# Kernel tuning notes

Hardware: AMD Instinct MI355X
Metric: run time of the kernel (lower is better)

## Reference

```python
import jax, jax.numpy as jnp
import numpy as np

B, T, E = 4, 1024, 1024
H, MULT = 16, 2
HD = E // H
SCALE = HD ** -0.5


def setup_inputs() -> dict:
    key = jax.random.key(0)
    ks = jax.random.split(key, 9)
    s = 0.02
    return {
        "hidden_states": jax.random.normal(ks[0], (B, T, E), jnp.float32),
        "attention_mask": jnp.zeros((B, 1, T, T), jnp.float32),
        "Wq": jax.random.normal(ks[1], (E, E), jnp.float32) * s,
        "bq": jnp.zeros((E,), jnp.float32),
        "Wk": jax.random.normal(ks[2], (MULT * E, E), jnp.float32) * s,
        "bk": jnp.zeros((MULT * E,), jnp.float32),
        "Wv": jax.random.normal(ks[3], (MULT * E, E), jnp.float32) * s,
        "bv": jnp.zeros((MULT * E,), jnp.float32),
        "Wo": jax.random.normal(ks[4], (E, E), jnp.float32) * s,
        "bo": jnp.zeros((E,), jnp.float32),
    }


def reference(hidden_states, attention_mask, Wq, bq, Wk, bk, Wv, bv, Wo, bo):
    x = hidden_states  # [B, T, E]
    # q projection, scaled
    q = (jnp.einsum("bte,fe->btf", x, Wq) + bq) * SCALE  # [B,T,E]
    q = q.reshape(B, T, H, HD).transpose(0, 2, 1, 3)      # [B,H,T,HD]
    # k/v project to multiplier-expanded dim, then _shape with seq_len=-1:
    # [B,T,MULT*E] -> view(B, T*MULT, H, HD) (torch view semantics) -> [B,H,T*MULT,HD]
    k = jnp.einsum("bte,fe->btf", x, Wk) + bk             # [B,T,MULT*E]
    k = k.reshape(B, T * MULT, H, HD).transpose(0, 2, 1, 3)
    v = jnp.einsum("bte,fe->btf", x, Wv) + bv
    v = v.reshape(B, T * MULT, H, HD).transpose(0, 2, 1, 3)

    S = T * MULT  # src_len; src_len0 = T
    attn = jnp.einsum("bhtd,bhsd->bhts", q, k)            # [B,H,T,S]
    # custom mask broadcast: view src as [MULT, src_len0] and add mask[:, :, :, None, :]
    attn = attn.reshape(B, H, T, MULT, T) + attention_mask[:, :, :, None, :]
    attn = attn.reshape(B, H, T, S)
    attn = jax.nn.softmax(attn, axis=-1)
    out = jnp.einsum("bhts,bhsd->bhtd", attn, v)          # [B,H,T,HD]
    out = out.transpose(0, 2, 1, 3).reshape(B, T, E)
    out = jnp.einsum("bte,fe->btf", out, Wo) + bo
    return out
```

## Files before the change

### kernel.cpp

```cpp
#include <hip/hip_runtime.h>
#include <math.h>

#define BB    4
#define TT    1024
#define EE    1024
#define HH    16
#define HDIM  64
#define SS    2048
#define MROWS 4096
#define SCALEQ 0.125f

typedef short  s8v  __attribute__((ext_vector_type(8)));
typedef float  f4v  __attribute__((ext_vector_type(4)));

__device__ __forceinline__ unsigned short f2bf(float f) {
    union { float f; unsigned u; } c; c.f = f;
    unsigned u = c.u + 0x7FFFu + ((c.u >> 16) & 1u);
    return (unsigned short)(u >> 16);
}
__device__ __forceinline__ float bf2f(unsigned short h) {
    union { unsigned u; float f; } c; c.u = ((unsigned)h) << 16;
    return c.f;
}

__device__ __forceinline__ void async16(const void* g, void* l) {
    __builtin_amdgcn_global_load_lds(
        (const __attribute__((address_space(1))) unsigned int*)g,
        (__attribute__((address_space(3))) unsigned int*)l,
        16, 0, 0);
}

__global__ __launch_bounds__(256) void cvt6_kernel(
    const float* __restrict__ x,  const float* __restrict__ wq,
    const float* __restrict__ wk, const float* __restrict__ wv,
    const float* __restrict__ wo, const float* __restrict__ mk,
    unsigned short* __restrict__ xb,  unsigned short* __restrict__ wqb,
    unsigned short* __restrict__ wkb, unsigned short* __restrict__ wvb,
    unsigned short* __restrict__ wob, unsigned short* __restrict__ mbb)
{
    const int total = 3670016;
    int i = blockIdx.x * 256 + threadIdx.x;
    const int stride = gridDim.x * 256;
    for (; i < total; i += stride) {
        const float* s; unsigned short* d; int off;
        if (i < 1048576)      { s = x;  d = xb;  off = i; }
        else if (i < 1310720) { s = wq; d = wqb; off = i - 1048576; }
        else if (i < 1835008) { s = wk; d = wkb; off = i - 1310720; }
        else if (i < 2359296) { s = wv; d = wvb; off = i - 1835008; }
        else if (i < 2621440) { s = wo; d = wob; off = i - 2359296; }
        else                  { s = mk; d = mbb; off = i - 2621440; }
        float4 v = ((const float4*)s)[off];
        ushort4 o;
        o.x = f2bf(v.x); o.y = f2bf(v.y); o.z = f2bf(v.z); o.w = f2bf(v.w);
        ((ushort4*)d)[off] = o;
    }
}

#define GEMM_KLOOP(Aptr, Wptr, Ksz)                                            \
    for (int k0 = 0; k0 < (Ksz); k0 += 32) {                                   \
        _Pragma("unroll")                                                      \
        for (int it = 0; it < 2; ++it) {                                       \
            int f = (it * 4 + w) * 64 + lane;                                  \
            int r = f >> 2, g = (f & 3) * 8;                                   \
            async16((Aptr) + (size_t)(m0 + r) * (Ksz) + k0 + g,                \
                    As + (it * 4 + w) * 512);                                  \
            async16((Wptr) + (size_t)(n0 + r) * (Ksz) + k0 + g,                \
                    Bs + (it * 4 + w) * 512);                                  \
        }                                                                      \
        __syncthreads();                                                       \
        s8v af[4], bf[4];                                                      \
        _Pragma("unroll")                                                      \
        for (int i = 0; i < 4; ++i)                                            \
            af[i] = *(const s8v*)(As + (wm + i * 16 + col16) * 32 + quad * 8); \
        _Pragma("unroll")                                                      \
        for (int j = 0; j < 4; ++j)                                            \
            bf[j] = *(const s8v*)(Bs + (wn + j * 16 + col16) * 32 + quad * 8); \
        _Pragma("unroll")                                                      \
        for (int i = 0; i < 4; ++i)                                            \
            _Pragma("unroll")                                                  \
            for (int j = 0; j < 4; ++j)                                        \
                acc[i][j] = __builtin_amdgcn_mfma_f32_16x16x32_bf16(           \
                    af[i], bf[j], acc[i][j], 0, 0, 0);                         \
        __syncthreads();                                                       \
    }

__global__ __launch_bounds__(256, 3) void gemm_qk_kernel(
    const unsigned short* __restrict__ X,  const unsigned short* __restrict__ Wq,
    const unsigned short* __restrict__ Wk, const float* __restrict__ bq,
    const float* __restrict__ bk, unsigned short* __restrict__ qp,
    unsigned short* __restrict__ kp)
{
    __shared__ __align__(16) unsigned short As[128 * 32];
    __shared__ __align__(16) unsigned short Bs[128 * 32];

    const int tid = threadIdx.x;
    const int lane = tid & 63, w = tid >> 6;
    const int wm = (w & 1) * 64, wn = (w >> 1) * 64;
    const int col16 = lane & 15, quad = lane >> 4;
    const int m0 = blockIdx.x * 128;
    const bool isQ = blockIdx.y < 8;
    const int n0 = blockIdx.y * 128;
    const unsigned short* Wrow = isQ ? Wq + (size_t)n0 * EE
                                     : Wk + (size_t)(n0 - EE) * EE;

    f4v acc[4][4];
#pragma unroll
    for (int i = 0; i < 4; ++i)
#pragma unroll
        for (int j = 0; j < 4; ++j) acc[i][j] = (f4v)0.0f;

    for (int k0 = 0; k0 < EE; k0 += 32) {
#pragma unroll
        for (int it = 0; it < 2; ++it) {
            int f = (it * 4 + w) * 64 + lane;
            int r = f >> 2, g = (f & 3) * 8;
            async16(X + (size_t)(m0 + r) * EE + k0 + g, As + (it * 4 + w) * 512);
            async16(Wrow + (size_t)r * EE + k0 + g, Bs + (it * 4 + w) * 512);
        }
        __syncthreads();
        s8v af[4], bf[4];
#pragma unroll
        for (int i = 0; i < 4; ++i)
            af[i] = *(const s8v*)(As + (wm + i * 16 + col16) * 32 + quad * 8);
#pragma unroll
        for (int j = 0; j < 4; ++j)
            bf[j] = *(const s8v*)(Bs + (wn + j * 16 + col16) * 32 + quad * 8);
#pragma unroll
        for (int i = 0; i < 4; ++i)
#pragma unroll
            for (int j = 0; j < 4; ++j)
                acc[i][j] = __builtin_amdgcn_mfma_f32_16x16x32_bf16(
                    af[i], bf[j], acc[i][j], 0, 0, 0);
        __syncthreads();
    }

#pragma unroll
    for (int j = 0; j < 4; ++j) {
        const int n = n0 + wn + j * 16 + col16;
        const float bn = isQ ? bq[n] : bk[n - EE];
#pragma unroll
        for (int i = 0; i < 4; ++i) {
            const int mb = m0 + wm + i * 16 + quad * 4;
#pragma unroll
            for (int r = 0; r < 4; ++r) {
                const int m = mb + r;
                float c = acc[i][j][r] + bn;
                if (isQ) {
                    qp[(size_t)m * EE + n] = f2bf(c * SCALEQ);
                } else {
                    const int nk = n - EE;
                    const int mm = nk >> 10, h = (nk >> 6) & 15, d = nk & 63;
                    const int b_ = m >> 10, t = m & 1023;
                    const int s = 2 * t + mm;
                    kp[((size_t)(b_ * HH + h) * SS + s) * HDIM + d] = f2bf(c);
                }
            }
        }
    }
}

template <int LAYOUT, int OUTF32, int Ksz, int Nsz>
__global__ __launch_bounds__(256, 3) void gemm_mfma_kernel(
    const unsigned short* __restrict__ A, const unsigned short* __restrict__ W,
    const float* __restrict__ bias, void* __restrict__ Cout, float alpha)
{
    __shared__ __align__(16) unsigned short As[128 * 32];
    __shared__ __align__(16) unsigned short Bs[128 * 32];

    const int tid = threadIdx.x;
    const int lane = tid & 63, w = tid >> 6;
    const int wm = (w & 1) * 64, wn = (w >> 1) * 64;
    const int col16 = lane & 15, quad = lane >> 4;
    const int m0 = blockIdx.x * 128;
    const int n0 = blockIdx.y * 128;

    f4v acc[4][4];
#pragma unroll
    for (int i = 0; i < 4; ++i)
#pragma unroll
        for (int j = 0; j < 4; ++j) acc[i][j] = (f4v)0.0f;

    GEMM_KLOOP(A, W, Ksz)

#pragma unroll
    for (int j = 0; j < 4; ++j) {
        const int n = n0 + wn + j * 16 + col16;
        const float bn = (LAYOUT == 2) ? 0.0f : bias[n];
#pragma unroll
        for (int i = 0; i < 4; ++i) {
            const int mb = m0 + wm + i * 16 + quad * 4;
#pragma unroll
            for (int r = 0; r < 4; ++r) {
                const int m = mb + r;
                float c = (acc[i][j][r] + ((LAYOUT == 2) ? bias[m] : bn)) * alpha;
                if (LAYOUT == 0) {
                    if (OUTF32) ((float*)Cout)[(size_t)m * Nsz + n] = c;
                    else ((unsigned short*)Cout)[(size_t)m * Nsz + n] = f2bf(c);
                } else {
                    const int mm = m >> 10, h = (m >> 6) & 15, d = m & 63;
                    const int b_ = n >> 10, t = n & 1023;
                    const int s = 2 * t + mm;
                    ((unsigned short*)Cout)[((size_t)(b_ * HH + h) * HDIM + d) * SS + s] = f2bf(c);
                }
            }
        }
    }
}

__global__ __launch_bounds__(256, 3) void attn_mfma2_kernel(
    const unsigned short* __restrict__ Q, const unsigned short* __restrict__ Kh,
    const unsigned short* __restrict__ Vt, const unsigned short* __restrict__ Mb,
    unsigned short* __restrict__ O)
{
    constexpr int PT = 68;
    __shared__ __align__(16) unsigned short Qs[64 * PT];
    __shared__ __align__(16) unsigned short K0[64 * PT];
    __shared__ __align__(16) unsigned short K1[64 * PT];
    __shared__ __align__(16) unsigned short V0[64 * PT];
    __shared__ __align__(16) unsigned short V1[64 * PT];
    __shared__ __align__(16) unsigned short Ms[64 * PT];

    const int tid = threadIdx.x;
    const int lane = tid & 63, w = tid >> 6;
    const int col16 = lane & 15, quad = lane >> 4;

    const int gid = blockIdx.x;
    const int v = gid & 7, j = gid >> 3;
    const int bh = v * 8 + (j >> 4);
    const int t0 = (j & 15) * 64;
    const int b_ = bh >> 4, h = bh & 15;

#pragma unroll
    for (int it = 0; it < 2; ++it) {
        int idx = tid + it * 256;
        int r = idx >> 3, c = (idx & 7) * 8;
        *(uint4*)(Qs + r * PT + c) =
            *(const uint4*)(Q + (size_t)(b_ * TT + t0 + r) * EE + h * HDIM + c);
    }

    f4v oacc[4];
#pragma unroll
    for (int jd = 0; jd < 4; ++jd) oacc[jd] = (f4v)0.0f;
    float mrun = -INFINITY, lrun = 0.0f;

    const unsigned short* Kb  = Kh + (size_t)bh * SS * HDIM;
    const unsigned short* Vb  = Vt + (size_t)bh * HDIM * SS;
    const unsigned short* Mbb = Mb + (size_t)b_ * TT * TT;
    const int myrow = (w * 16 + col16) * PT;

    for (int it16 = 0; it16 < 16; ++it16) {
        const int t2b = it16 * 64;
        __syncthreads();
#pragma unroll
        for (int st = 0; st < 2; ++st) {
            int idx = tid + st * 256;
            int r = idx >> 3, c = (idx & 7) * 8;
            *(uint4*)(K0 + r * PT + c) = *(const uint4*)(Kb + (size_t)(t2b + r) * HDIM + c);
            *(uint4*)(K1 + r * PT + c) = *(const uint4*)(Kb + (size_t)(1024 + t2b + r) * HDIM + c);
            *(uint4*)(V0 + r * PT + c) = *(const uint4*)(Vb + (size_t)r * SS + t2b + c);
            *(uint4*)(V1 + r * PT + c) = *(const uint4*)(Vb + (size_t)r * SS + 1024 + t2b + c);
            *(uint4*)(Ms + r * PT + c) = *(const uint4*)(Mbb + (size_t)(t0 + r) * TT + t2b + c);
        }
        __syncthreads();

        f4v s0acc[4], s1acc[4];
#pragma unroll
        for (int js = 0; js < 4; ++js) { s0acc[js] = (f4v)0.0f; s1acc[js] = (f4v)0.0f; }
#pragma unroll
        for (int ks = 0; ks < 2; ++ks) {
            s8v bq_ = *(const s8v*)(Qs + myrow + ks * 32 + quad * 8);
#pragma unroll
            for (int js = 0; js < 4; ++js) {
                s8v ak0 = *(const s8v*)(K0 + (js * 16 + col16) * PT + ks * 32 + quad * 8);
                s8v ak1 = *(const s8v*)(K1 + (js * 16 + col16) * PT + ks * 32 + quad * 8);
                s0acc[js] = __builtin_amdgcn_mfma_f32_16x16x32_bf16(ak0, bq_, s0acc[js], 0, 0, 0);
                s1acc[js] = __builtin_amdgcn_mfma_f32_16x16x32_bf16(ak1, bq_, s1acc[js], 0, 0, 0);
            }
        }

#pragma unroll
        for (int js = 0; js < 4; ++js) {
            uint2 mm = *(const uint2*)(Ms + myrow + js * 16 + quad * 4);
            float m0f = bf2f((unsigned short)(mm.x & 0xffff));
            float m1f = bf2f((unsigned short)(mm.x >> 16));
            float m2f = bf2f((unsigned short)(mm.y & 0xffff));
            float m3f = bf2f((unsigned short)(mm.y >> 16));
            s0acc[js][0] += m0f; s1acc[js][0] += m0f;
            s0acc[js][1] += m1f; s1acc[js][1] += m1f;
            s0acc[js][2] += m2f; s1acc[js][2] += m2f;
            s0acc[js][3] += m3f; s1acc[js][3] += m3f;
        }

        float tmax = -INFINITY;
#pragma unroll
        for (int js = 0; js < 4; ++js)
#pragma unroll
            for (int r = 0; r < 4; ++r)
                tmax = fmaxf(tmax, fmaxf(s0acc[js][r], s1acc[js][r]));
        tmax = fmaxf(tmax, __shfl_xor(tmax, 16));
        tmax = fmaxf(tmax, __shfl_xor(tmax, 32));
        const float mnew = fmaxf(mrun, tmax);
        const float scl = __expf(mrun - mnew);
        float rs = 0.0f;
#pragma unroll
        for (int js = 0; js < 4; ++js)
#pragma unroll
            for (int r = 0; r < 4; ++r) {
                float p0 = __expf(s0acc[js][r] - mnew);
                float p1 = __expf(s1acc[js][r] - mnew);
                s0acc[js][r] = p0; s1acc[js][r] = p1;
                rs += p0 + p1;
            }
        rs += __shfl_xor(rs, 16);
        rs += __shfl_xor(rs, 32);
        lrun = lrun * scl + rs;
        mrun = mnew;

        float sclr[4];
#pragma unroll
        for (int r = 0; r < 4; ++r) sclr[r] = __shfl(scl, quad * 4 + r);
#pragma unroll
        for (int jd = 0; jd < 4; ++jd)
#pragma unroll
            for (int r = 0; r < 4; ++r) oacc[jd][r] *= sclr[r];

        __syncthreads();

#pragma unroll
        for (int js = 0; js < 4; ++js) {
            unsigned p01 = (unsigned)f2bf(s0acc[js][0]) | ((unsigned)f2bf(s0acc[js][1]) << 16);
            unsigned p23 = (unsigned)f2bf(s0acc[js][2]) | ((unsigned)f2bf(s0acc[js][3]) << 16);
            *(uint2*)(K0 + myrow + js * 16 + quad * 4) = make_uint2(p01, p23);
            p01 = (unsigned)f2bf(s1acc[js][0]) | ((unsigned)f2bf(s1acc[js][1]) << 16);
            p23 = (unsigned)f2bf(s1acc[js][2]) | ((unsigned)f2bf(s1acc[js][3]) << 16);
            *(uint2*)(K1 + myrow + js * 16 + quad * 4) = make_uint2(p01, p23);
        }
        __syncthreads();

#pragma unroll
        for (int ks = 0; ks < 2; ++ks) {
            s8v p0 = *(const s8v*)(K0 + myrow + ks * 32 + quad * 8);
            s8v p1 = *(const s8v*)(K1 + myrow + ks * 32 + quad * 8);
#pragma unroll
            for (int jd = 0; jd < 4; ++jd) {
                s8v v0_ = *(const s8v*)(V0 + (jd * 16 + col16) * PT + ks * 32 + quad * 8);
                s8v v1_ = *(const s8v*)(V1 + (jd * 16 + col16) * PT + ks * 32 + quad * 8);
                oacc[jd] = __builtin_amdgcn_mfma_f32_16x16x32_bf16(p0, v0_, oacc[jd], 0, 0, 0);
                oacc[jd] = __builtin_amdgcn_mfma_f32_16x16x32_bf16(p1, v1_, oacc[jd], 0, 0, 0);
            }
        }
    }

    const float inv = 1.0f / lrun;
    float invr[4];
#pragma unroll
    for (int r = 0; r < 4; ++r) invr[r] = __shfl(inv, quad * 4 + r);
#pragma unroll
    for (int r = 0; r < 4; ++r) {
        const int t = t0 + w * 16 + quad * 4 + r;
#pragma unroll
        for (int jd = 0; jd < 4; ++jd)
            O[(size_t)(b_ * TT + t) * EE + h * HDIM + jd * 16 + col16] =
                f2bf(oacc[jd][r] * invr[r]);
    }
}

extern "C" void kernel_launch(void* const* d_in, const int* in_sizes, int n_in,
                              void* d_out, int out_size, void* d_ws, size_t ws_size,
                              hipStream_t stream)
{
    (void)in_sizes; (void)n_in; (void)out_size; (void)ws_size;

    const float* x    = (const float*)d_in[0];
    const float* mask = (const float*)d_in[1];
    const float* Wq   = (const float*)d_in[2];
    const float* bq   = (const float*)d_in[3];
    const float* Wk   = (const float*)d_in[4];
    const float* bk   = (const float*)d_in[5];
    const float* Wv   = (const float*)d_in[6];
    const float* bv   = (const float*)d_in[7];
    const float* Wo   = (const float*)d_in[8];
    const float* bo   = (const float*)d_in[9];
    float* out = (float*)d_out;

    unsigned short* xb  = (unsigned short*)d_ws;
    unsigned short* wqb = xb  + (size_t)MROWS * EE;
    unsigned short* wkb = wqb + (size_t)EE * EE;
    unsigned short* wvb = wkb + (size_t)2 * EE * EE;
    unsigned short* wob = wvb + (size_t)2 * EE * EE;
    unsigned short* mb  = wob + (size_t)EE * EE;
    unsigned short* qp  = mb  + (size_t)BB * TT * TT;
    unsigned short* kp  = qp  + (size_t)MROWS * EE;
    unsigned short* vt  = kp  + (size_t)BB * HH * SS * HDIM;
    unsigned short* ao  = vt  + (size_t)BB * HH * SS * HDIM;

    dim3 blk(256);

    cvt6_kernel<<<4096, blk, 0, stream>>>(x, Wq, Wk, Wv, Wo, mask,
                                          xb, wqb, wkb, wvb, wob, mb);
    gemm_qk_kernel<<<dim3(32, 24), blk, 0, stream>>>(xb, wqb, wkb, bq, bk, qp, kp);
    gemm_mfma_kernel<2, 0, EE, MROWS><<<dim3(16, 32), blk, 0, stream>>>(
        wvb, xb, bv, vt, 1.0f);
    attn_mfma2_kernel<<<dim3(1024), blk, 0, stream>>>(qp, kp, vt, mb, ao);
    gemm_mfma_kernel<0, 1, EE, EE><<<dim3(32, 8), blk, 0, stream>>>(
        ao, wob, bo, out, 1.0f);
}
```

Baseline: 287.0 us.

## Use exp2 softmax with lazy rescaling, register Q and mask, less LDS

Folds log2(e) into the Q scale and the mask conversion so the softmax can use native exp2. The running max is only updated when a new tile exceeds it by more than a threshold, and the row sum is kept per lane and reduced once at the end. Q fragments and mask values now load straight into registers instead of going through shared memory. That frees LDS and lets occupancy rise to 4 blocks per CU. Packed bf16 conversion uses an inline cvt_pk instruction; the trade-off is that lazy rescaling lets exponents grow up to 2^10 before renormalising.

```diff
diff --git a/kernel.cpp b/kernel.cpp
--- a/kernel.cpp
+++ b/kernel.cpp
@@ -8,7 +8,8 @@
 #define HDIM  64
 #define SS    2048
 #define MROWS 4096
-#define SCALEQ 0.125f
+#define QSCALE 0.18033688011112f
+#define LOG2E  1.4426950408889634f
 
 typedef short  s8v  __attribute__((ext_vector_type(8)));
 typedef float  f4v  __attribute__((ext_vector_type(4)));
@@ -18,9 +19,11 @@
     unsigned u = c.u + 0x7FFFu + ((c.u >> 16) & 1u);
     return (unsigned short)(u >> 16);
 }
-__device__ __forceinline__ float bf2f(unsigned short h) {
-    union { unsigned u; float f; } c; c.u = ((unsigned)h) << 16;
-    return c.f;
+__device__ __forceinline__ float bflo(unsigned u) {
+    union { unsigned u; float f; } c; c.u = u << 16; return c.f;
+}
+__device__ __forceinline__ float bfhi(unsigned u) {
+    union { unsigned u; float f; } c; c.u = u & 0xffff0000u; return c.f;
 }
 
 __device__ __forceinline__ void async16(const void* g, void* l) {
@@ -42,16 +45,17 @@
     int i = blockIdx.x * 256 + threadIdx.x;
     const int stride = gridDim.x * 256;
     for (; i < total; i += stride) {
-        const float* s; unsigned short* d; int off;
+        const float* s; unsigned short* d; int off; float sc = 1.0f;
         if (i < 1048576)      { s = x;  d = xb;  off = i; }
         else if (i < 1310720) { s = wq; d = wqb; off = i - 1048576; }
         else if (i < 1835008) { s = wk; d = wkb; off = i - 1310720; }
         else if (i < 2359296) { s = wv; d = wvb; off = i - 1835008; }
         else if (i < 2621440) { s = wo; d = wob; off = i - 2359296; }
-        else                  { s = mk; d = mbb; off = i - 2621440; }
+        else                  { s = mk; d = mbb; off = i - 2621440; sc = LOG2E; }
         float4 v = ((const float4*)s)[off];
         ushort4 o;
-        o.x = f2bf(v.x); o.y = f2bf(v.y); o.z = f2bf(v.z); o.w = f2bf(v.w);
+        o.x = f2bf(v.x * sc); o.y = f2bf(v.y * sc);
+        o.z = f2bf(v.z * sc); o.w = f2bf(v.w * sc);
         ((ushort4*)d)[off] = o;
     }
 }
@@ -146,7 +150,7 @@
                 const int m = mb + r;
                 float c = acc[i][j][r] + bn;
                 if (isQ) {
-                    qp[(size_t)m * EE + n] = f2bf(c * SCALEQ);
+                    qp[(size_t)m * EE + n] = f2bf(c * QSCALE);
                 } else {
                     const int nk = n - EE;
                     const int mm = nk >> 10, h = (nk >> 6) & 15, d = nk & 63;
@@ -207,18 +211,16 @@
     }
 }
 
-__global__ __launch_bounds__(256, 3) void attn_mfma2_kernel(
+__global__ __launch_bounds__(256, 4) void attn_mfma3_kernel(
     const unsigned short* __restrict__ Q, const unsigned short* __restrict__ Kh,
     const unsigned short* __restrict__ Vt, const unsigned short* __restrict__ Mb,
     unsigned short* __restrict__ O)
 {
     constexpr int PT = 68;
-    __shared__ __align__(16) unsigned short Qs[64 * PT];
     __shared__ __align__(16) unsigned short K0[64 * PT];
     __shared__ __align__(16) unsigned short K1[64 * PT];
     __shared__ __align__(16) unsigned short V0[64 * PT];
     __shared__ __align__(16) unsigned short V1[64 * PT];
-    __shared__ __align__(16) unsigned short Ms[64 * PT];
 
     const int tid = threadIdx.x;
     const int lane = tid & 63, w = tid >> 6;
@@ -230,26 +232,31 @@
     const int t0 = (j & 15) * 64;
     const int b_ = bh >> 4, h = bh & 15;
 
-#pragma unroll
-    for (int it = 0; it < 2; ++it) {
-        int idx = tid + it * 256;
-        int r = idx >> 3, c = (idx & 7) * 8;
-        *(uint4*)(Qs + r * PT + c) =
-            *(const uint4*)(Q + (size_t)(b_ * TT + t0 + r) * EE + h * HDIM + c);
-    }
+    const unsigned short* Qrow =
+        Q + (size_t)(b_ * TT + t0 + w * 16 + col16) * EE + h * HDIM;
+    const s8v qf0 = *(const s8v*)(Qrow + quad * 8);
+    const s8v qf1 = *(const s8v*)(Qrow + 32 + quad * 8);
 
     f4v oacc[4];
 #pragma unroll
     for (int jd = 0; jd < 4; ++jd) oacc[jd] = (f4v)0.0f;
-    float mrun = -INFINITY, lrun = 0.0f;
-
-    const unsigned short* Kb  = Kh + (size_t)bh * SS * HDIM;
-    const unsigned short* Vb  = Vt + (size_t)bh * HDIM * SS;
-    const unsigned short* Mbb = Mb + (size_t)b_ * TT * TT;
+    float mrun = -INFINITY;
+    f4v l4 = (f4v)0.0f;
+
+    const unsigned short* Kb   = Kh + (size_t)bh * SS * HDIM;
+    const unsigned short* Vb   = Vt + (size_t)bh * HDIM * SS;
+    const unsigned short* Mrow = Mb + (size_t)b_ * TT * TT
+                               + (size_t)(t0 + w * 16 + col16) * TT;
     const int myrow = (w * 16 + col16) * PT;
 
     for (int it16 = 0; it16 < 16; ++it16) {
         const int t2b = it16 * 64;
+
+        uint2 mm[4];
+#pragma unroll
+        for (int js = 0; js < 4; ++js)
+            mm[js] = *(const uint2*)(Mrow + t2b + js * 16 + quad * 4);
+
         __syncthreads();
 #pragma unroll
         for (int st = 0; st < 2; ++st) {
@@ -259,16 +266,20 @@
             *(uint4*)(K1 + r * PT + c) = *(const uint4*)(Kb + (size_t)(1024 + t2b + r) * HDIM + c);
             *(uint4*)(V0 + r * PT + c) = *(const uint4*)(Vb + (size_t)r * SS + t2b + c);
             *(uint4*)(V1 + r * PT + c) = *(const uint4*)(Vb + (size_t)r * SS + 1024 + t2b + c);
-            *(uint4*)(Ms + r * PT + c) = *(const uint4*)(Mbb + (size_t)(t0 + r) * TT + t2b + c);
         }
         __syncthreads();
 
         f4v s0acc[4], s1acc[4];
 #pragma unroll
-        for (int js = 0; js < 4; ++js) { s0acc[js] = (f4v)0.0f; s1acc[js] = (f4v)0.0f; }
+        for (int js = 0; js < 4; ++js) {
+            f4v mv;
+            mv[0] = bflo(mm[js].x); mv[1] = bfhi(mm[js].x);
+            mv[2] = bflo(mm[js].y); mv[3] = bfhi(mm[js].y);
+            s0acc[js] = mv; s1acc[js] = mv;
+        }
 #pragma unroll
         for (int ks = 0; ks < 2; ++ks) {
-            s8v bq_ = *(const s8v*)(Qs + myrow + ks * 32 + quad * 8);
+            const s8v bq_ = ks ? qf1 : qf0;
 #pragma unroll
             for (int js = 0; js < 4; ++js) {
                 s8v ak0 = *(const s8v*)(K0 + (js * 16 + col16) * PT + ks * 32 + quad * 8);
@@ -278,62 +289,56 @@
             }
         }
 
+        float tm0 = fmaxf(fmaxf(s0acc[0][0], s0acc[0][1]), fmaxf(s0acc[0][2], s0acc[0][3]));
+        float tm1 = fmaxf(fmaxf(s0acc[1][0], s0acc[1][1]), fmaxf(s0acc[1][2], s0acc[1][3]));
+        float tm2 = fmaxf(fmaxf(s0acc[2][0], s0acc[2][1]), fmaxf(s0acc[2][2], s0acc[2][3]));
+        float tm3 = fmaxf(fmaxf(s0acc[3][0], s0acc[3][1]), fmaxf(s0acc[3][2], s0acc[3][3]));
+        float tn0 = fmaxf(fmaxf(s1acc[0][0], s1acc[0][1]), fmaxf(s1acc[0][2], s1acc[0][3]));
+        float tn1 = fmaxf(fmaxf(s1acc[1][0], s1acc[1][1]), fmaxf(s1acc[1][2], s1acc[1][3]));
+        float tn2 = fmaxf(fmaxf(s1acc[2][0], s1acc[2][1]), fmaxf(s1acc[2][2], s1acc[2][3]));
+        float tn3 = fmaxf(fmaxf(s1acc[3][0], s1acc[3][1]), fmaxf(s1acc[3][2], s1acc[3][3]));
+        float tmax = fmaxf(fmaxf(fmaxf(tm0, tm1), fmaxf(tm2, tm3)),
+                           fmaxf(fmaxf(tn0, tn1), fmaxf(tn2, tn3)));
+
+        if (!__all(tmax - mrun <= 10.0f)) {
+            float tfull = fmaxf(tmax, __shfl_xor(tmax, 16));
+            tfull = fmaxf(tfull, __shfl_xor(tfull, 32));
+            const float mnew = fmaxf(mrun, tfull);
+            const float scl = __builtin_amdgcn_exp2f(mrun - mnew);
+            l4 *= scl;
+            float sclr[4];
+#pragma unroll
+            for (int r = 0; r < 4; ++r) sclr[r] = __shfl(scl, quad * 4 + r);
+#pragma unroll
+            for (int jd = 0; jd < 4; ++jd)
+#pragma unroll
+                for (int r = 0; r < 4; ++r) oacc[jd][r] *= sclr[r];
+            mrun = mnew;
+        }
+
+        unsigned pk0[8], pk1[8];
 #pragma unroll
         for (int js = 0; js < 4; ++js) {
-            uint2 mm = *(const uint2*)(Ms + myrow + js * 16 + quad * 4);
-            float m0f = bf2f((unsigned short)(mm.x & 0xffff));
-            float m1f = bf2f((unsigned short)(mm.x >> 16));
-            float m2f = bf2f((unsigned short)(mm.y & 0xffff));
-            float m3f = bf2f((unsigned short)(mm.y >> 16));
-            s0acc[js][0] += m0f; s1acc[js][0] += m0f;
-            s0acc[js][1] += m1f; s1acc[js][1] += m1f;
-            s0acc[js][2] += m2f; s1acc[js][2] += m2f;
-            s0acc[js][3] += m3f; s1acc[js][3] += m3f;
-        }
-
-        float tmax = -INFINITY;
-#pragma unroll
-        for (int js = 0; js < 4; ++js)
-#pragma unroll
-            for (int r = 0; r < 4; ++r)
-                tmax = fmaxf(tmax, fmaxf(s0acc[js][r], s1acc[js][r]));
-        tmax = fmaxf(tmax, __shfl_xor(tmax, 16));
-        tmax = fmaxf(tmax, __shfl_xor(tmax, 32));
-        const float mnew = fmaxf(mrun, tmax);
-        const float scl = __expf(mrun - mnew);
-        float rs = 0.0f;
-#pragma unroll
-        for (int js = 0; js < 4; ++js)
+            f4v p0 = s0acc[js] - mrun;
+            f4v p1 = s1acc[js] - mrun;
 #pragma unroll
             for (int r = 0; r < 4; ++r) {
-                float p0 = __expf(s0acc[js][r] - mnew);
-                float p1 = __expf(s1acc[js][r] - mnew);
-                s0acc[js][r] = p0; s1acc[js][r] = p1;
-                rs += p0 + p1;
+                p0[r] = __builtin_amdgcn_exp2f(p0[r]);
+                p1[r] = __builtin_amdgcn_exp2f(p1[r]);
             }
-        rs += __shfl_xor(rs, 16);
-        rs += __shfl_xor(rs, 32);
-        lrun = lrun * scl + rs;
-        mrun = mnew;
-
-        float sclr[4];
-#pragma unroll
-        for (int r = 0; r < 4; ++r) sclr[r] = __shfl(scl, quad * 4 + r);
-#pragma unroll
-        for (int jd = 0; jd < 4; ++jd)
-#pragma unroll
-            for (int r = 0; r < 4; ++r) oacc[jd][r] *= sclr[r];
+            l4 += p0 + p1;
+            __asm__("v_cvt_pk_bf16_f32 %0, %1, %2" : "=v"(pk0[js*2])   : "v"(p0[0]), "v"(p0[1]));
+            __asm__("v_cvt_pk_bf16_f32 %0, %1, %2" : "=v"(pk0[js*2+1]) : "v"(p0[2]), "v"(p0[3]));
+            __asm__("v_cvt_pk_bf16_f32 %0, %1, %2" : "=v"(pk1[js*2])   : "v"(p1[0]), "v"(p1[1]));
+            __asm__("v_cvt_pk_bf16_f32 %0, %1, %2" : "=v"(pk1[js*2+1]) : "v"(p1[2]), "v"(p1[3]));
+        }
 
         __syncthreads();
 
 #pragma unroll
         for (int js = 0; js < 4; ++js) {
-            unsigned p01 = (unsigned)f2bf(s0acc[js][0]) | ((unsigned)f2bf(s0acc[js][1]) << 16);
-            unsigned p23 = (unsigned)f2bf(s0acc[js][2]) | ((unsigned)f2bf(s0acc[js][3]) << 16);
-            *(uint2*)(K0 + myrow + js * 16 + quad * 4) = make_uint2(p01, p23);
-            p01 = (unsigned)f2bf(s1acc[js][0]) | ((unsigned)f2bf(s1acc[js][1]) << 16);
-            p23 = (unsigned)f2bf(s1acc[js][2]) | ((unsigned)f2bf(s1acc[js][3]) << 16);
-            *(uint2*)(K1 + myrow + js * 16 + quad * 4) = make_uint2(p01, p23);
+            *(uint2*)(K0 + myrow + js * 16 + quad * 4) = make_uint2(pk0[js*2], pk0[js*2+1]);
+            *(uint2*)(K1 + myrow + js * 16 + quad * 4) = make_uint2(pk1[js*2], pk1[js*2+1]);
         }
         __syncthreads();
 
@@ -351,7 +356,10 @@
         }
     }
 
-    const float inv = 1.0f / lrun;
+    float lr = l4[0] + l4[1] + l4[2] + l4[3];
+    lr += __shfl_xor(lr, 16);
+    lr += __shfl_xor(lr, 32);
+    const float inv = 1.0f / lr;
     float invr[4];
 #pragma unroll
     for (int r = 0; r < 4; ++r) invr[r] = __shfl(inv, quad * 4 + r);
@@ -401,7 +409,7 @@
     gemm_qk_kernel<<<dim3(32, 24), blk, 0, stream>>>(xb, wqb, wkb, bq, bk, qp, kp);
     gemm_mfma_kernel<2, 0, EE, MROWS><<<dim3(16, 32), blk, 0, stream>>>(
         wvb, xb, bv, vt, 1.0f);
-    attn_mfma2_kernel<<<dim3(1024), blk, 0, stream>>>(qp, kp, vt, mb, ao);
+    attn_mfma3_kernel<<<dim3(1024), blk, 0, stream>>>(qp, kp, vt, mb, ao);
     gemm_mfma_kernel<0, 1, EE, EE><<<dim3(32, 8), blk, 0, stream>>>(
         ao, wob, bo, out, 1.0f);
 }
```

Measured after the change: 268.2 us. -6.6%, faster.
